# Kernel tuning notes

Hardware: AMD Instinct MI355X
Metric: run time of the kernel (lower is better)

Reference implementation:

```python
import jax, jax.numpy as jnp
import numpy as np

D = 512      # d_model
H = 8        # n_heads
DK = D // H  # head dim
DFF = 4 * D  # d_ff
E = 3        # encoder layers
PRED = 256   # pred_len
C_OUT = 64


def _ln(x, g, b):
    m = jnp.mean(x, axis=-1, keepdims=True)
    v = jnp.var(x, axis=-1, keepdims=True)
    return (x - m) / jnp.sqrt(v + 1e-5) * g + b


def _attn(q_in, kv_in, Wq, bq, Wk, bk, Wv, bv, Wo, bo, causal):
    B, L, _ = q_in.shape
    S = kv_in.shape[1]
    q = (q_in @ Wq + bq).reshape(B, L, H, DK)
    k = (kv_in @ Wk + bk).reshape(B, S, H, DK)
    v = (kv_in @ Wv + bv).reshape(B, S, H, DK)
    scores = jnp.einsum('blhe,bshe->bhls', q, k)  # [B,H,L,S]
    if causal:
        mask = jnp.triu(jnp.ones((L, S), dtype=bool), k=1)
        scores = jnp.where(mask, -jnp.inf, scores)
    scale = 1.0 / jnp.sqrt(jnp.asarray(DK, scores.dtype))
    A = jax.nn.softmax(scores * scale, axis=-1)
    out = jnp.einsum('bhls,bshd->blhd', A, v).reshape(B, L, H * DK)
    return out @ Wo + bo


def _gelu(x):
    return jax.nn.gelu(x, approximate=False)  # torch F.gelu is exact erf


def setup_inputs() -> dict:
    ks = iter(jax.random.split(jax.random.key(0), 80))
    r = lambda *s: jax.random.normal(next(ks), s, jnp.float32) * 0.02
    inp = {}
    inp['x_dec'] = jax.random.normal(next(ks), (8, 512, D), jnp.float32)
    inp['x_enc'] = jax.random.normal(next(ks), (8, 1024, D), jnp.float32)
    # encoder params, stacked over layers
    for nm in ['Wq', 'Wk', 'Wv', 'Wo']:
        inp[f'enc_{nm}'] = r(E, D, D)
        inp[f'enc_b{nm[1].lower()}'] = r(E, D)
    inp['enc_W1'] = r(E, D, DFF); inp['enc_b1'] = r(E, DFF)
    inp['enc_W2'] = r(E, DFF, D); inp['enc_b2'] = r(E, D)
    inp['enc_g1'] = jnp.ones((E, D)); inp['enc_beta1'] = jnp.zeros((E, D))
    inp['enc_g2'] = jnp.ones((E, D)); inp['enc_beta2'] = jnp.zeros((E, D))
    inp['enc_ng'] = jnp.ones((D,)); inp['enc_nbeta'] = jnp.zeros((D,))
    # decoder (single layer) params
    for p in ['s', 'c']:
        for nm in ['Wq', 'Wk', 'Wv', 'Wo']:
            inp[f'dec_{p}{nm}'] = r(D, D)
            inp[f'dec_{p}b{nm[1].lower()}'] = r(D)
    inp['dec_W1'] = r(D, DFF); inp['dec_b1'] = r(DFF)
    inp['dec_W2'] = r(DFF, D); inp['dec_b2'] = r(D)
    inp['dec_g1'] = jnp.ones((D,)); inp['dec_beta1'] = jnp.zeros((D,))
    inp['dec_g2'] = jnp.ones((D,)); inp['dec_beta2'] = jnp.zeros((D,))
    inp['dec_g3'] = jnp.ones((D,)); inp['dec_beta3'] = jnp.zeros((D,))
    inp['dec_ng'] = jnp.ones((D,)); inp['dec_nbeta'] = jnp.zeros((D,))
    inp['proj_W'] = r(D, C_OUT); inp['proj_b'] = r(C_OUT)
    return inp


def reference(x_dec, x_enc,
              enc_Wq, enc_bq, enc_Wk, enc_bk, enc_Wv, enc_bv, enc_Wo, enc_bo,
              enc_W1, enc_b1, enc_W2, enc_b2,
              enc_g1, enc_beta1, enc_g2, enc_beta2, enc_ng, enc_nbeta,
              dec_sWq, dec_sbq, dec_sWk, dec_sbk, dec_sWv, dec_sbv, dec_sWo, dec_sbo,
              dec_cWq, dec_cbq, dec_cWk, dec_cbk, dec_cWv, dec_cbv, dec_cWo, dec_cbo,
              dec_W1, dec_b1, dec_W2, dec_b2,
              dec_g1, dec_beta1, dec_g2, dec_beta2, dec_g3, dec_beta3,
              dec_ng, dec_nbeta, proj_W, proj_b):
    # ----- encoder (non-causal self-attn, eval mode: dropout = identity) -----
    x = x_enc
    for l in range(E):
        a = _attn(x, x, enc_Wq[l], enc_bq[l], enc_Wk[l], enc_bk[l],
                  enc_Wv[l], enc_bv[l], enc_Wo[l], enc_bo[l], causal=False)
        x = _ln(x + a, enc_g1[l], enc_beta1[l])
        y = _gelu(x @ enc_W1[l] + enc_b1[l]) @ enc_W2[l] + enc_b2[l]
        x = _ln(x + y, enc_g2[l], enc_beta2[l])
    enc_out = _ln(x, enc_ng, enc_nbeta)
    # ----- decoder (causal self-attn + cross-attn) -----
    x = x_dec
    a = _attn(x, x, dec_sWq, dec_sbq, dec_sWk, dec_sbk,
              dec_sWv, dec_sbv, dec_sWo, dec_sbo, causal=True)
    x = _ln(x + a, dec_g1, dec_beta1)
    a = _attn(x, enc_out, dec_cWq, dec_cbq, dec_cWk, dec_cbk,
              dec_cWv, dec_cbv, dec_cWo, dec_cbo, causal=False)
    x = _ln(x + a, dec_g2, dec_beta2)
    y = _gelu(x @ dec_W1 + dec_b1) @ dec_W2 + dec_b2
    x = _ln(x + y, dec_g3, dec_beta3)
    x = _ln(x, dec_ng, dec_nbeta)
    out = x @ proj_W + proj_b
    return out[:, -PRED:, :]
```

## Files before the change

### kernel.cpp

```cpp
#include <hip/hip_runtime.h>
#include <cstddef>

typedef __bf16 bf16;
typedef __bf16 bf16x8 __attribute__((ext_vector_type(8)));
typedef float f32x4 __attribute__((ext_vector_type(4)));

#define D 512
#define DFF 2048
#define MFMA __builtin_amdgcn_mfma_f32_16x16x32_bf16

__device__ __forceinline__ float load_any(const void* p, size_t i, int f) {
  return f ? ((const float*)p)[i] : (float)((const bf16*)p)[i];
}

__global__ void detect_dtype(const unsigned* __restrict__ x, int* flag) {
  __shared__ int cnt;
  if (threadIdx.x == 0) cnt = 0;
  __syncthreads();
  int local = 0;
  for (int i = threadIdx.x; i < 32768; i += 256) {
    unsigned e = (x[i] >> 7) & 0xFFu;
    if (e >= 160u) local++;
  }
  atomicAdd(&cnt, local);
  __syncthreads();
  if (threadIdx.x == 0) *flag = (cnt > 100) ? 1 : 0;
}

__global__ __launch_bounds__(256)
void conv_to_bf16(const void* __restrict__ src, bf16* __restrict__ dst, int n,
                  const int* __restrict__ flag) {
  const int f = *flag;
  for (int i = blockIdx.x * 256 + threadIdx.x; i < n; i += gridDim.x * 256)
    dst[i] = (bf16)load_any(src, i, f);
}

struct CDesc { const void* src; unsigned long long off; bf16* dst; int n; int pad; };
struct CPack { CDesc d[40]; };
__global__ __launch_bounds__(256)
void conv_batch(CPack P, const int* __restrict__ flag) {
  const CDesc& c = P.d[blockIdx.z];
  const int f = *flag;
  for (int i = blockIdx.x * 256 + threadIdx.x; i < c.n; i += gridDim.x * 256)
    c.dst[i] = (bf16)load_any(c.src, c.off + i, f);
}

struct TDesc { const void* src; unsigned long long off; bf16* dst; };
struct TPack { TDesc d[20]; };
__global__ __launch_bounds__(256)
void transpose_b(TPack P, int Kd, int Nd, const int* __restrict__ flag) {
  __shared__ bf16 tile[64][65];
  const TDesc& t = P.d[blockIdx.z];
  const int f = *flag;
  int tx = threadIdx.x & 63, ty = threadIdx.x >> 6;
  int nb = blockIdx.x * 64, kb = blockIdx.y * 64;
  #pragma unroll
  for (int r = ty; r < 64; r += 4)
    tile[r][tx] = (bf16)load_any(t.src, t.off + (size_t)(kb + r) * Nd + nb + tx, f);
  __syncthreads();
  #pragma unroll
  for (int r = ty; r < 64; r += 4)
    t.dst[(size_t)(nb + r) * Kd + kb + tx] = tile[tx][r];
}

__global__ __launch_bounds__(256)
void prep_kv(const bf16* __restrict__ K, const bf16* __restrict__ V,
             bf16* __restrict__ Kf, bf16* __restrict__ Vf, int S)
{
  __shared__ bf16 tile[64][72];
  const int kt = blockIdx.x, h = blockIdx.y, b = blockIdx.z;
  const int t = threadIdx.x;
  const int r = t >> 2, g = t & 3;
  const size_t srcrow = ((size_t)(b * S + kt * 64 + r)) * D + h * 64 + g * 16;
  const size_t bh = (size_t)(b * 8 + h);
  const size_t tbase = (bh * (S >> 6) + kt) * 4096;

  bf16x8 k0 = *(const bf16x8*)(K + srcrow);
  bf16x8 k1 = *(const bf16x8*)(K + srcrow + 8);
  const int nt = r >> 4, m15 = r & 15;
  const int c = g >> 1, qq = (g & 1) * 2;
  *(bf16x8*)(Kf + tbase + (((nt * 2 + c) * 64) + qq * 16 + m15) * 8)       = k0;
  *(bf16x8*)(Kf + tbase + (((nt * 2 + c) * 64) + (qq + 1) * 16 + m15) * 8) = k1;

  bf16x8 v0 = *(const bf16x8*)(V + srcrow);
  bf16x8 v1 = *(const bf16x8*)(V + srcrow + 8);
  #pragma unroll
  for (int u = 0; u < 8; u++) {
    tile[g * 16 + u][r]     = v0[u];
    tile[g * 16 + 8 + u][r] = v1[u];
  }
  __syncthreads();
  #pragma unroll
  for (int s = 0; s < 2; s++) {
    int i = t * 2 + s;
    int lane = i & 63, ntc = i >> 6;
    int vq = lane >> 4, vm = lane & 15;
    int vnt = ntc >> 1, vc = ntc & 1;
    bf16x8 o = *(const bf16x8*)(&tile[vnt * 16 + vm][vc * 32 + vq * 8]);
    *(bf16x8*)(Vf + tbase + (size_t)i * 8) = o;
  }
}

__device__ __forceinline__ void gload_lds16(const bf16* g, bf16* l) {
  __builtin_amdgcn_global_load_lds((const __attribute__((address_space(1))) void*)g,
                                   (__attribute__((address_space(3))) void*)l,
                                   16, 0, 0);
}

__global__ __launch_bounds__(256, 2)
void gemm_bt(const bf16* __restrict__ A, const bf16* __restrict__ BT,
             const bf16* __restrict__ bias, bf16* __restrict__ C,
             int M, int N, int K, int act)
{
  __shared__ bf16 As[128 * 32];
  __shared__ bf16 Bs[128 * 32];
  const int tid = threadIdx.x;
  const int bm = blockIdx.y, bn = blockIdx.x;
  const int wid = tid >> 6, lane = tid & 63;
  const int wm = (wid >> 1) << 6, wn = (wid & 1) << 6;
  const int l15 = lane & 15, q = lane >> 4;

  f32x4 acc[4][4] = {};

  const bf16* ag = A + (size_t)(bm * 128 + (tid >> 2)) * K + (tid & 3) * 8;
  const bf16* bg = BT + (size_t)(bn * 128 + (tid >> 2)) * K + (tid & 3) * 8;
  const size_t rstep = (size_t)64 * K;
  bf16* asl = As + tid * 8;
  bf16* bsl = Bs + tid * 8;

  for (int k0 = 0; k0 < K; k0 += 32) {
    __syncthreads();
    gload_lds16(ag + k0,          asl);
    gload_lds16(ag + k0 + rstep,  asl + 256 * 8);
    gload_lds16(bg + k0,          bsl);
    gload_lds16(bg + k0 + rstep,  bsl + 256 * 8);
    __syncthreads();

    bf16x8 af[4], bq[4];
    #pragma unroll
    for (int i = 0; i < 4; i++)
      af[i] = *(const bf16x8*)(As + (wm + i * 16 + l15) * 32 + q * 8);
    #pragma unroll
    for (int j = 0; j < 4; j++)
      bq[j] = *(const bf16x8*)(Bs + (wn + j * 16 + l15) * 32 + q * 8);
    #pragma unroll
    for (int i = 0; i < 4; i++)
      #pragma unroll
      for (int j = 0; j < 4; j++)
        acc[i][j] = MFMA(af[i], bq[j], acc[i][j], 0, 0, 0);
  }

  #pragma unroll
  for (int j = 0; j < 4; j++) {
    int gcol = bn * 128 + wn + j * 16 + l15;
    float bv = (float)bias[gcol];
    #pragma unroll
    for (int i = 0; i < 4; i++) {
      int grow = bm * 128 + wm + i * 16 + q * 4;
      #pragma unroll
      for (int r = 0; r < 4; r++) {
        float v = acc[i][j][r] + bv;
        if (act == 1) v = 0.5f * v * (1.0f + erff(v * 0.70710678118654752f));
        C[(size_t)(grow + r) * N + gcol] = (bf16)v;
      }
    }
  }
}

__global__ __launch_bounds__(256, 2)
void gemm_seg(const bf16* __restrict__ A, const bf16* __restrict__ BT,
              const bf16* __restrict__ bias,
              bf16* __restrict__ O0, bf16* __restrict__ O1, bf16* __restrict__ O2,
              int M, int K)
{
  __shared__ bf16 As[128 * 32];
  __shared__ bf16 Bs[128 * 32];
  const int tid = threadIdx.x;
  const int bm = blockIdx.y, bn = blockIdx.x;
  const int wid = tid >> 6, lane = tid & 63;
  const int wm = (wid >> 1) << 6, wn = (wid & 1) << 6;
  const int l15 = lane & 15, q = lane >> 4;

  f32x4 acc[4][4] = {};

  const bf16* ag = A + (size_t)(bm * 128 + (tid >> 2)) * K + (tid & 3) * 8;
  const bf16* bg = BT + (size_t)(bn * 128 + (tid >> 2)) * K + (tid & 3) * 8;
  const size_t rstep = (size_t)64 * K;
  bf16* asl = As + tid * 8;
  bf16* bsl = Bs + tid * 8;

  for (int k0 = 0; k0 < K; k0 += 32) {
    __syncthreads();
    gload_lds16(ag + k0,          asl);
    gload_lds16(ag + k0 + rstep,  asl + 256 * 8);
    gload_lds16(bg + k0,          bsl);
    gload_lds16(bg + k0 + rstep,  bsl + 256 * 8);
    __syncthreads();

    bf16x8 af[4], bq[4];
    #pragma unroll
    for (int i = 0; i < 4; i++)
      af[i] = *(const bf16x8*)(As + (wm + i * 16 + l15) * 32 + q * 8);
    #pragma unroll
    for (int j = 0; j < 4; j++)
      bq[j] = *(const bf16x8*)(Bs + (wn + j * 16 + l15) * 32 + q * 8);
    #pragma unroll
    for (int i = 0; i < 4; i++)
      #pragma unroll
      for (int j = 0; j < 4; j++)
        acc[i][j] = MFMA(af[i], bq[j], acc[i][j], 0, 0, 0);
  }

  const int seg = (bn * 128) >> 9;
  bf16* Cp = (seg == 0) ? O0 : ((seg == 1) ? O1 : O2);
  const int colb = seg << 9;

  #pragma unroll
  for (int j = 0; j < 4; j++) {
    int gcol = bn * 128 + wn + j * 16 + l15;
    float bv = (float)bias[gcol];
    int lcol = gcol - colb;
    #pragma unroll
    for (int i = 0; i < 4; i++) {
      int grow = bm * 128 + wm + i * 16 + q * 4;
      #pragma unroll
      for (int r = 0; r < 4; r++)
        Cp[(size_t)(grow + r) * 512 + lcol] = (bf16)(acc[i][j][r] + bv);
    }
  }
}

__global__ __launch_bounds__(256, 2)
void flash_attn(const bf16* __restrict__ Q, const bf16* __restrict__ Kf,
                const bf16* __restrict__ Vf, bf16* __restrict__ O,
                int L, int S, int causal)
{
  __shared__ bf16 PL[4][32 * 72];
  const int tid = threadIdx.x, wid = tid >> 6, lane = tid & 63;
  const int m15 = lane & 15, q = lane >> 4;
  const int b = blockIdx.z, h = blockIdx.y;
  const int wq = blockIdx.x * 128 + wid * 32;

  bf16x8 aq[2][2];
  #pragma unroll
  for (int qh = 0; qh < 2; qh++) {
    const bf16* qp = Q + ((size_t)(b * L + wq + qh * 16 + m15)) * D + h * 64 + q * 8;
    aq[qh][0] = *(const bf16x8*)(qp);
    aq[qh][1] = *(const bf16x8*)(qp + 32);
  }
  const size_t bh = (size_t)(b * 8 + h);
  const bf16* kfb = Kf + bh * ((size_t)S * 64);
  const bf16* vfb = Vf + bh * ((size_t)S * 64);

  f32x4 acco[2][4] = {};
  float ls[2][4] = {};

  const int ktmax = causal ? ((wq + 95) >> 6) : (S >> 6);

  bf16x8 kf[4][2];
  #pragma unroll
  for (int nt = 0; nt < 4; nt++)
    #pragma unroll
    for (int c = 0; c < 2; c++)
      kf[nt][c] = *(const bf16x8*)(kfb + ((nt * 2 + c) * 64 + lane) * 8);

  bf16* pl = &PL[wid][0];

  for (int kt = 0; kt < ktmax; kt++) {
    bf16x8 vf[4][2];
    const bf16* vc = vfb + (size_t)kt * 4096;
    #pragma unroll
    for (int nt = 0; nt < 4; nt++)
      #pragma unroll
      for (int c = 0; c < 2; c++)
        vf[nt][c] = *(const bf16x8*)(vc + ((nt * 2 + c) * 64 + lane) * 8);

    f32x4 sc[2][4];
    #pragma unroll
    for (int qh = 0; qh < 2; qh++)
      #pragma unroll
      for (int nt = 0; nt < 4; nt++) {
        f32x4 z = {};
        z = MFMA(aq[qh][0], kf[nt][0], z, 0, 0, 0);
        z = MFMA(aq[qh][1], kf[nt][1], z, 0, 0, 0);
        sc[qh][nt] = z;
      }

    {
      const int knext = (kt + 1 < ktmax) ? kt + 1 : kt;
      const bf16* kc = kfb + (size_t)knext * 4096;
      #pragma unroll
      for (int nt = 0; nt < 4; nt++)
        #pragma unroll
        for (int c = 0; c < 2; c++)
          kf[nt][c] = *(const bf16x8*)(kc + ((nt * 2 + c) * 64 + lane) * 8);
    }

    const bool mask = causal && (kt == ktmax - 1);
    #pragma unroll
    for (int qh = 0; qh < 2; qh++)
      #pragma unroll
      for (int nt = 0; nt < 4; nt++)
        #pragma unroll
        for (int r = 0; r < 4; r++) {
          float s = sc[qh][nt][r] * 0.125f;
          if (mask) {
            int kg = kt * 64 + nt * 16 + m15;
            int qg = wq + qh * 16 + q * 4 + r;
            if (kg > qg) s = -1e30f;
          }
          float p = __expf(s);
          ls[qh][r] += p;
          pl[(qh * 16 + q * 4 + r) * 72 + nt * 16 + m15] = (bf16)p;
        }

    #pragma unroll
    for (int qh = 0; qh < 2; qh++) {
      bf16x8 pa0 = *(const bf16x8*)(pl + (qh * 16 + m15) * 72 + q * 8);
      bf16x8 pa1 = *(const bf16x8*)(pl + (qh * 16 + m15) * 72 + 32 + q * 8);
      #pragma unroll
      for (int nt = 0; nt < 4; nt++) {
        acco[qh][nt] = MFMA(pa0, vf[nt][0], acco[qh][nt], 0, 0, 0);
        acco[qh][nt] = MFMA(pa1, vf[nt][1], acco[qh][nt], 0, 0, 0);
      }
    }
  }

  #pragma unroll
  for (int qh = 0; qh < 2; qh++)
    #pragma unroll
    for (int r = 0; r < 4; r++) {
      float v = ls[qh][r];
      v += __shfl_xor(v, 1); v += __shfl_xor(v, 2);
      v += __shfl_xor(v, 4); v += __shfl_xor(v, 8);
      ls[qh][r] = 1.0f / v;
    }

  #pragma unroll
  for (int qh = 0; qh < 2; qh++)
    #pragma unroll
    for (int nt = 0; nt < 4; nt++)
      #pragma unroll
      for (int r = 0; r < 4; r++)
        O[((size_t)(b * L + wq + qh * 16 + q * 4 + r)) * D + h * 64 + nt * 16 + m15] =
            (bf16)(acco[qh][nt][r] * ls[qh][r]);
}

__global__ __launch_bounds__(256)
void add_ln(const bf16* __restrict__ X, const bf16* __restrict__ R,
            const bf16* __restrict__ g, const bf16* __restrict__ be,
            bf16* __restrict__ Y, int hasR)
{
  __shared__ float red[4];
  const int row = blockIdx.x, tid = threadIdx.x;
  const bf16* x = X + (size_t)row * D;
  float v0 = (float)x[tid], v1 = (float)x[tid + 256];
  if (hasR) {
    const bf16* r = R + (size_t)row * D;
    v0 += (float)r[tid]; v1 += (float)r[tid + 256];
  }
  float s = v0 + v1;
  #pragma unroll
  for (int o = 32; o > 0; o >>= 1) s += __shfl_down(s, o);
  if ((tid & 63) == 0) red[tid >> 6] = s;
  __syncthreads();
  const float mean = (red[0] + red[1] + red[2] + red[3]) * (1.0f / 512.0f);
  __syncthreads();
  const float d0 = v0 - mean, d1 = v1 - mean;
  float sq = d0 * d0 + d1 * d1;
  #pragma unroll
  for (int o = 32; o > 0; o >>= 1) sq += __shfl_down(sq, o);
  if ((tid & 63) == 0) red[tid >> 6] = sq;
  __syncthreads();
  const float var = (red[0] + red[1] + red[2] + red[3]) * (1.0f / 512.0f);
  const float rstd = rsqrtf(var + 1e-5f);
  bf16* y = Y + (size_t)row * D;
  y[tid]       = (bf16)(d0 * rstd * (float)g[tid]       + (float)be[tid]);
  y[tid + 256] = (bf16)(d1 * rstd * (float)g[tid + 256] + (float)be[tid + 256]);
}

__global__ __launch_bounds__(256)
void proj_out(const bf16* __restrict__ X, const bf16* __restrict__ Wp,
              const bf16* __restrict__ bp, void* __restrict__ out,
              const int* __restrict__ flag)
{
  __shared__ float part[4][64];
  const int rb = blockIdx.x;
  const int b = rb >> 8, t = rb & 255;
  const int tid = threadIdx.x;
  const bf16* x = X + ((size_t)(b * 512 + 256 + t)) * D;
  const int c = tid & 63, seg = tid >> 6;
  float acc = 0.f;
  for (int k = seg * 128; k < seg * 128 + 128; k++)
    acc += (float)x[k] * (float)Wp[(size_t)k * 64 + c];
  part[seg][c] = acc;
  __syncthreads();
  if (tid < 64) {
    float v = part[0][tid] + part[1][tid] + part[2][tid] + part[3][tid] + (float)bp[tid];
    size_t idx = (size_t)rb * 64 + tid;
    if (*flag) ((float*)out)[idx] = v;
    else       ((bf16*)out)[idx] = (bf16)v;
  }
}

extern "C" void kernel_launch(void* const* d_in, const int* in_sizes, int n_in,
                              void* d_out, int out_size, void* d_ws, size_t ws_size,
                              hipStream_t stream)
{
  (void)in_sizes; (void)n_in; (void)out_size; (void)ws_size;

  char* wsb = (char*)d_ws;
  int* flag = (int*)wsb;
  bf16* w = (bf16*)(wsb + 256);
  size_t off = 0;
  auto alloc = [&](size_t n) { bf16* p = w + off; off += n; return p; };

  bf16* eQKVT = alloc(3 * (size_t)1536 * D);
  bf16* eWoT  = alloc(3 * (size_t)D * D);
  bf16* eW1T  = alloc(3 * (size_t)D * DFF);
  bf16* eW2T  = alloc(3 * (size_t)D * DFF);
  bf16* dQKVT = alloc((size_t)1536 * D);
  bf16* sWoT  = alloc((size_t)D * D);
  bf16* cWqT  = alloc((size_t)D * D);
  bf16* cKVT  = alloc((size_t)1024 * D);
  bf16* cWoT  = alloc((size_t)D * D);
  bf16* dW1T  = alloc((size_t)D * DFF);
  bf16* dW2T  = alloc((size_t)D * DFF);
  bf16* pW    = alloc((size_t)D * 64);
  bf16* e_qkvb  = alloc(3 * 1536);
  bf16* d_sqkvb = alloc(1536);
  bf16* d_ckvb  = alloc(1024);
  bf16* c_ebo = alloc(3 * D);
  bf16* c_eb1 = alloc(3 * DFF); bf16* c_eb2 = alloc(3 * D);
  bf16* c_eg1 = alloc(3 * D);   bf16* c_ebe1 = alloc(3 * D);
  bf16* c_eg2 = alloc(3 * D);   bf16* c_ebe2 = alloc(3 * D);
  bf16* c_eng = alloc(D);       bf16* c_enb = alloc(D);
  bf16* c_dsbo = alloc(D);
  bf16* c_dcbq = alloc(D);      bf16* c_dcbo = alloc(D);
  bf16* c_db1 = alloc(DFF);     bf16* c_db2 = alloc(D);
  bf16* c_dg1 = alloc(D);  bf16* c_dbe1 = alloc(D);
  bf16* c_dg2 = alloc(D);  bf16* c_dbe2 = alloc(D);
  bf16* c_dg3 = alloc(D);  bf16* c_dbe3 = alloc(D);
  bf16* c_dng = alloc(D);  bf16* c_dnb = alloc(D);
  bf16* c_pb  = alloc(64);
  bf16* xe   = alloc((size_t)8192 * D);
  bf16* enco = alloc((size_t)8192 * D);
  bf16* xd0  = alloc((size_t)4096 * D);
  bf16* xd   = alloc((size_t)4096 * D);
  bf16* qb   = alloc((size_t)8192 * D);
  bf16* kb   = alloc((size_t)8192 * D);
  bf16* vb   = alloc((size_t)8192 * D);
  bf16* t0   = alloc((size_t)8192 * D);
  bf16* t1   = alloc((size_t)8192 * D);
  bf16* mid  = qb;

  const dim3 tb(256);

  detect_dtype<<<dim3(1), tb, 0, stream>>>((const unsigned*)d_in[1], flag);

  conv_to_bf16<<<dim3(1024), tb, 0, stream>>>(d_in[1], xe, 8 * 1024 * D, flag);
  conv_to_bf16<<<dim3(1024), tb, 0, stream>>>(d_in[0], xd0, 8 * 512 * D, flag);

  {
    CPack P{};
    int n = 0;
    auto add = [&](int idx, unsigned long long o, bf16* dst, int cnt) {
      P.d[n++] = {d_in[idx], o, dst, cnt, 0};
    };
    add(9, 0, c_ebo, 1536);
    add(11, 0, c_eb1, 6144);  add(13, 0, c_eb2, 1536);
    add(14, 0, c_eg1, 1536);  add(15, 0, c_ebe1, 1536);
    add(16, 0, c_eg2, 1536);  add(17, 0, c_ebe2, 1536);
    add(18, 0, c_eng, 512);   add(19, 0, c_enb, 512);
    add(27, 0, c_dsbo, 512);
    add(29, 0, c_dcbq, 512);  add(35, 0, c_dcbo, 512);
    add(37, 0, c_db1, 2048);  add(39, 0, c_db2, 512);
    add(40, 0, c_dg1, 512);   add(41, 0, c_dbe1, 512);
    add(42, 0, c_dg2, 512);   add(43, 0, c_dbe2, 512);
    add(44, 0, c_dg3, 512);   add(45, 0, c_dbe3, 512);
    add(46, 0, c_dng, 512);   add(47, 0, c_dnb, 512);
    add(48, 0, pW, D * 64);   add(49, 0, c_pb, 64);
    for (int l = 0; l < 3; l++) {
      add(3, (unsigned long long)l * D, e_qkvb + l * 1536, 512);
      add(5, (unsigned long long)l * D, e_qkvb + l * 1536 + 512, 512);
      add(7, (unsigned long long)l * D, e_qkvb + l * 1536 + 1024, 512);
    }
    add(21, 0, d_sqkvb, 512); add(23, 0, d_sqkvb + 512, 512); add(25, 0, d_sqkvb + 1024, 512);
    add(31, 0, d_ckvb, 512);  add(33, 0, d_ckvb + 512, 512);
    conv_batch<<<dim3(24, 1, n), tb, 0, stream>>>(P, flag);
  }

  {
    TPack P{};
    int n = 0;
    for (int l = 0; l < 3; l++) {
      unsigned long long wo = (unsigned long long)l * D * D;
      bf16* dst = eQKVT + (size_t)l * 1536 * D;
      P.d[n++] = {d_in[2], wo, dst};
      P.d[n++] = {d_in[4], wo, dst + 512 * D};
      P.d[n++] = {d_in[6], wo, dst + 1024 * D};
      P.d[n++] = {d_in[8], wo, eWoT + wo};
    }
    P.d[n++] = {d_in[20], 0, dQKVT};
    P.d[n++] = {d_in[22], 0, dQKVT + 512 * D};
    P.d[n++] = {d_in[24], 0, dQKVT + 1024 * D};
    P.d[n++] = {d_in[26], 0, sWoT};
    P.d[n++] = {d_in[28], 0, cWqT};
    P.d[n++] = {d_in[30], 0, cKVT};
    P.d[n++] = {d_in[32], 0, cKVT + 512 * D};
    P.d[n++] = {d_in[34], 0, cWoT};
    transpose_b<<<dim3(8, 8, n), tb, 0, stream>>>(P, D, D, flag);
  }
  {
    TPack P{};
    for (int l = 0; l < 3; l++)
      P.d[l] = {d_in[10], (unsigned long long)l * D * DFF, eW1T + (size_t)l * D * DFF};
    P.d[3] = {d_in[36], 0, dW1T};
    transpose_b<<<dim3(32, 8, 4), tb, 0, stream>>>(P, D, DFF, flag);
  }
  {
    TPack P{};
    for (int l = 0; l < 3; l++)
      P.d[l] = {d_in[12], (unsigned long long)l * D * DFF, eW2T + (size_t)l * D * DFF};
    P.d[3] = {d_in[38], 0, dW2T};
    transpose_b<<<dim3(8, 32, 4), tb, 0, stream>>>(P, DFF, D, flag);
  }

  auto G = [&](const bf16* A, const bf16* BT, const bf16* bias, bf16* C,
               int M, int N, int K, int act) {
    gemm_bt<<<dim3(N / 128, M / 128), tb, 0, stream>>>(A, BT, bias, C, M, N, K, act);
  };
  auto GS = [&](const bf16* A, const bf16* BT, const bf16* bias,
                bf16* O0, bf16* O1, bf16* O2, int M, int N, int K) {
    gemm_seg<<<dim3(N / 128, M / 128), tb, 0, stream>>>(A, BT, bias, O0, O1, O2, M, K);
  };
  auto PK = [&](const bf16* Kp, const bf16* Vp, bf16* Kfp, bf16* Vfp, int S) {
    prep_kv<<<dim3(S / 64, 8, 8), tb, 0, stream>>>(Kp, Vp, Kfp, Vfp, S);
  };
  auto FA = [&](const bf16* Qp, const bf16* Kfp, const bf16* Vfp, bf16* Op,
                int L, int S, int causal) {
    flash_attn<<<dim3(L / 128, 8, 8), tb, 0, stream>>>(Qp, Kfp, Vfp, Op, L, S, causal);
  };

  const int Me = 8192;
  for (int l = 0; l < 3; l++) {
    const size_t wo = (size_t)l * D * D, fo = (size_t)l * D * DFF;
    GS(xe, eQKVT + (size_t)l * 1536 * D, e_qkvb + l * 1536, qb, kb, vb, Me, 1536, D);
    PK(kb, vb, t1, enco, 1024);
    FA(qb, t1, enco, t0, 1024, 1024, 0);
    G(t0, eWoT + wo, c_ebo + l * D, t1, Me, D, D, 0);
    add_ln<<<dim3(8192), tb, 0, stream>>>(t1, xe, c_eg1 + l * D, c_ebe1 + l * D, xe, 1);
    G(xe, eW1T + fo, c_eb1 + l * DFF, mid, Me, DFF, D, 1);
    G(mid, eW2T + fo, c_eb2 + l * D, t1, Me, D, DFF, 0);
    add_ln<<<dim3(8192), tb, 0, stream>>>(t1, xe, c_eg2 + l * D, c_ebe2 + l * D, xe, 1);
  }
  add_ln<<<dim3(8192), tb, 0, stream>>>(xe, nullptr, c_eng, c_enb, enco, 0);

  const int Md = 4096;
  GS(xd0, dQKVT, d_sqkvb, qb, kb, vb, Md, 1536, D);
  PK(kb, vb, t1, xd, 512);
  FA(qb, t1, xd, t0, 512, 512, 1);
  G(t0, sWoT, c_dsbo, t1, Md, D, D, 0);
  add_ln<<<dim3(4096), tb, 0, stream>>>(t1, xd0, c_dg1, c_dbe1, xd, 1);
  G(xd, cWqT, c_dcbq, qb, Md, D, D, 0);
  GS(enco, cKVT, d_ckvb, kb, vb, nullptr, Me, 1024, D);
  PK(kb, vb, t1, enco, 1024);
  FA(qb, t1, enco, t0, 512, 1024, 0);
  G(t0, cWoT, c_dcbo, t1, Md, D, D, 0);
  add_ln<<<dim3(4096), tb, 0, stream>>>(t1, xd, c_dg2, c_dbe2, xd, 1);
  G(xd, dW1T, c_db1, mid, Md, DFF, D, 1);
  G(mid, dW2T, c_db2, t1, Md, D, DFF, 0);
  add_ln<<<dim3(4096), tb, 0, stream>>>(t1, xd, c_dg3, c_dbe3, xd, 1);
  add_ln<<<dim3(4096), tb, 0, stream>>>(xd, nullptr, c_dng, c_dnb, xd, 0);
  proj_out<<<dim3(2048), tb, 0, stream>>>(xd, pW, c_pb, d_out, flag);
}
```

Baseline: 1.035 ms.

## Split-K for N=512 GEMMs with partial sums fused into add-LN, plus XCD block swizzle

Output-projection and FFN-down GEMMs (N=512) now use a two-way split-K kernel that writes two bf16 partial results. The add+layernorm kernel sums both partials, so no separate reduction pass is needed. The aim is to double the block count of these narrow GEMMs and fill more CUs. Separately, GEMM block indices are remapped so consecutive blocks spread across the 8 XCDs, to improve L2 reuse of A rows. The cost is an extra partial-buffer write and read per GEMM, and partials rounded to bf16 before summing slightly changes numerics.

Measured after the change: 950.9 us. 1.09x faster.

```diff
diff --git a/kernel.cpp b/kernel.cpp
--- a/kernel.cpp
+++ b/kernel.cpp
@@ -107,6 +107,17 @@
                                    16, 0, 0);
 }
 
+__device__ __forceinline__ void swizzle_bm_bn(int& bm, int& bn) {
+  int lin = blockIdx.y * gridDim.x + blockIdx.x;
+  if ((gridDim.y & 7) == 0) {
+    int xcd = lin & 7, j = lin >> 3;
+    bn = j % gridDim.x;
+    bm = xcd + 8 * (j / gridDim.x);
+  } else {
+    bn = blockIdx.x; bm = blockIdx.y;
+  }
+}
+
 __global__ __launch_bounds__(256, 2)
 void gemm_bt(const bf16* __restrict__ A, const bf16* __restrict__ BT,
              const bf16* __restrict__ bias, bf16* __restrict__ C,
@@ -115,7 +126,7 @@
   __shared__ bf16 As[128 * 32];
   __shared__ bf16 Bs[128 * 32];
   const int tid = threadIdx.x;
-  const int bm = blockIdx.y, bn = blockIdx.x;
+  int bm, bn; swizzle_bm_bn(bm, bn);
   const int wid = tid >> 6, lane = tid & 63;
   const int wm = (wid >> 1) << 6, wn = (wid & 1) << 6;
   const int l15 = lane & 15, q = lane >> 4;
@@ -168,6 +179,66 @@
 }
 
 __global__ __launch_bounds__(256, 2)
+void gemm_ks(const bf16* __restrict__ A, const bf16* __restrict__ BT,
+             const bf16* __restrict__ bias, bf16* __restrict__ P0,
+             bf16* __restrict__ P1, int M, int N, int K)
+{
+  __shared__ bf16 As[128 * 32];
+  __shared__ bf16 Bs[128 * 32];
+  const int tid = threadIdx.x;
+  int bm, bnl; swizzle_bm_bn(bm, bnl);
+  const int bn = bnl >> 1, split = bnl & 1;
+  const int Kh = K >> 1, kbase = split * Kh;
+  const int wid = tid >> 6, lane = tid & 63;
+  const int wm = (wid >> 1) << 6, wn = (wid & 1) << 6;
+  const int l15 = lane & 15, q = lane >> 4;
+
+  f32x4 acc[4][4] = {};
+
+  const bf16* ag = A + (size_t)(bm * 128 + (tid >> 2)) * K + kbase + (tid & 3) * 8;
+  const bf16* bg = BT + (size_t)(bn * 128 + (tid >> 2)) * K + kbase + (tid & 3) * 8;
+  const size_t rstep = (size_t)64 * K;
+  bf16* asl = As + tid * 8;
+  bf16* bsl = Bs + tid * 8;
+
+  for (int k0 = 0; k0 < Kh; k0 += 32) {
+    __syncthreads();
+    gload_lds16(ag + k0,          asl);
+    gload_lds16(ag + k0 + rstep,  asl + 256 * 8);
+    gload_lds16(bg + k0,          bsl);
+    gload_lds16(bg + k0 + rstep,  bsl + 256 * 8);
+    __syncthreads();
+
+    bf16x8 af[4], bq[4];
+    #pragma unroll
+    for (int i = 0; i < 4; i++)
+      af[i] = *(const bf16x8*)(As + (wm + i * 16 + l15) * 32 + q * 8);
+    #pragma unroll
+    for (int j = 0; j < 4; j++)
+      bq[j] = *(const bf16x8*)(Bs + (wn + j * 16 + l15) * 32 + q * 8);
+    #pragma unroll
+    for (int i = 0; i < 4; i++)
+      #pragma unroll
+      for (int j = 0; j < 4; j++)
+        acc[i][j] = MFMA(af[i], bq[j], acc[i][j], 0, 0, 0);
+  }
+
+  bf16* Cp = split ? P1 : P0;
+  #pragma unroll
+  for (int j = 0; j < 4; j++) {
+    int gcol = bn * 128 + wn + j * 16 + l15;
+    float bv = split ? 0.0f : (float)bias[gcol];
+    #pragma unroll
+    for (int i = 0; i < 4; i++) {
+      int grow = bm * 128 + wm + i * 16 + q * 4;
+      #pragma unroll
+      for (int r = 0; r < 4; r++)
+        Cp[(size_t)(grow + r) * 512 + gcol] = (bf16)(acc[i][j][r] + bv);
+    }
+  }
+}
+
+__global__ __launch_bounds__(256, 2)
 void gemm_seg(const bf16* __restrict__ A, const bf16* __restrict__ BT,
               const bf16* __restrict__ bias,
               bf16* __restrict__ O0, bf16* __restrict__ O1, bf16* __restrict__ O2,
@@ -176,7 +247,7 @@
   __shared__ bf16 As[128 * 32];
   __shared__ bf16 Bs[128 * 32];
   const int tid = threadIdx.x;
-  const int bm = blockIdx.y, bn = blockIdx.x;
+  int bm, bn; swizzle_bm_bn(bm, bn);
   const int wid = tid >> 6, lane = tid & 63;
   const int wm = (wid >> 1) << 6, wn = (wid & 1) << 6;
   const int l15 = lane & 15, q = lane >> 4;
@@ -347,14 +418,19 @@
 }
 
 __global__ __launch_bounds__(256)
-void add_ln(const bf16* __restrict__ X, const bf16* __restrict__ R,
+void add_ln(const bf16* __restrict__ X0, const bf16* __restrict__ X1,
+            const bf16* __restrict__ R,
             const bf16* __restrict__ g, const bf16* __restrict__ be,
             bf16* __restrict__ Y, int hasR)
 {
   __shared__ float red[4];
   const int row = blockIdx.x, tid = threadIdx.x;
-  const bf16* x = X + (size_t)row * D;
+  const bf16* x = X0 + (size_t)row * D;
   float v0 = (float)x[tid], v1 = (float)x[tid + 256];
+  if (X1 != nullptr) {
+    const bf16* p = X1 + (size_t)row * D;
+    v0 += (float)p[tid]; v1 += (float)p[tid + 256];
+  }
   if (hasR) {
     const bf16* r = R + (size_t)row * D;
     v0 += (float)r[tid]; v1 += (float)r[tid + 256];
@@ -530,6 +606,10 @@
                int M, int N, int K, int act) {
     gemm_bt<<<dim3(N / 128, M / 128), tb, 0, stream>>>(A, BT, bias, C, M, N, K, act);
   };
+  auto KS = [&](const bf16* A, const bf16* BT, const bf16* bias,
+                bf16* P0, bf16* P1, int M, int K) {
+    gemm_ks<<<dim3(8, M / 128), tb, 0, stream>>>(A, BT, bias, P0, P1, M, 512, K);
+  };
   auto GS = [&](const bf16* A, const bf16* BT, const bf16* bias,
                 bf16* O0, bf16* O1, bf16* O2, int M, int N, int K) {
     gemm_seg<<<dim3(N / 128, M / 128), tb, 0, stream>>>(A, BT, bias, O0, O1, O2, M, K);
@@ -541,6 +621,10 @@
                 int L, int S, int causal) {
     flash_attn<<<dim3(L / 128, 8, 8), tb, 0, stream>>>(Qp, Kfp, Vfp, Op, L, S, causal);
   };
+  auto LN = [&](const bf16* X0, const bf16* X1, const bf16* R,
+                const bf16* g, const bf16* be, bf16* Y, int hasR, int M) {
+    add_ln<<<dim3(M), tb, 0, stream>>>(X0, X1, R, g, be, Y, hasR);
+  };
 
   const int Me = 8192;
   for (int l = 0; l < 3; l++) {
@@ -548,29 +632,29 @@
     GS(xe, eQKVT + (size_t)l * 1536 * D, e_qkvb + l * 1536, qb, kb, vb, Me, 1536, D);
     PK(kb, vb, t1, enco, 1024);
     FA(qb, t1, enco, t0, 1024, 1024, 0);
-    G(t0, eWoT + wo, c_ebo + l * D, t1, Me, D, D, 0);
-    add_ln<<<dim3(8192), tb, 0, stream>>>(t1, xe, c_eg1 + l * D, c_ebe1 + l * D, xe, 1);
+    KS(t0, eWoT + wo, c_ebo + l * D, t1, enco, Me, 512);
+    LN(t1, enco, xe, c_eg1 + l * D, c_ebe1 + l * D, xe, 1, Me);
     G(xe, eW1T + fo, c_eb1 + l * DFF, mid, Me, DFF, D, 1);
-    G(mid, eW2T + fo, c_eb2 + l * D, t1, Me, D, DFF, 0);
-    add_ln<<<dim3(8192), tb, 0, stream>>>(t1, xe, c_eg2 + l * D, c_ebe2 + l * D, xe, 1);
-  }
-  add_ln<<<dim3(8192), tb, 0, stream>>>(xe, nullptr, c_eng, c_enb, enco, 0);
+    KS(mid, eW2T + fo, c_eb2 + l * D, t1, enco, Me, 2048);
+    LN(t1, enco, xe, c_eg2 + l * D, c_ebe2 + l * D, xe, 1, Me);
+  }
+  LN(xe, nullptr, nullptr, c_eng, c_enb, enco, 0, Me);
 
   const int Md = 4096;
   GS(xd0, dQKVT, d_sqkvb, qb, kb, vb, Md, 1536, D);
   PK(kb, vb, t1, xd, 512);
   FA(qb, t1, xd, t0, 512, 512, 1);
-  G(t0, sWoT, c_dsbo, t1, Md, D, D, 0);
-  add_ln<<<dim3(4096), tb, 0, stream>>>(t1, xd0, c_dg1, c_dbe1, xd, 1);
+  KS(t0, sWoT, c_dsbo, t1, vb, Md, 512);
+  LN(t1, vb, xd0, c_dg1, c_dbe1, xd, 1, Md);
   G(xd, cWqT, c_dcbq, qb, Md, D, D, 0);
   GS(enco, cKVT, d_ckvb, kb, vb, nullptr, Me, 1024, D);
   PK(kb, vb, t1, enco, 1024);
   FA(qb, t1, enco, t0, 512, 1024, 0);
-  G(t0, cWoT, c_dcbo, t1, Md, D, D, 0);
-  add_ln<<<dim3(4096), tb, 0, stream>>>(t1, xd, c_dg2, c_dbe2, xd, 1);
+  KS(t0, cWoT, c_dcbo, t1, vb, Md, 512);
+  LN(t1, vb, xd, c_dg2, c_dbe2, xd, 1, Md);
   G(xd, dW1T, c_db1, mid, Md, DFF, D, 1);
-  G(mid, dW2T, c_db2, t1, Md, D, DFF, 0);
-  add_ln<<<dim3(4096), tb, 0, stream>>>(t1, xd, c_dg3, c_dbe3, xd, 1);
-  add_ln<<<dim3(4096), tb, 0, stream>>>(xd, nullptr, c_dng, c_dnb, xd, 0);
+  KS(mid, dW2T, c_db2, t1, vb, Md, 2048);
+  LN(t1, vb, xd, c_dg3, c_dbe3, xd, 1, Md);
+  LN(xd, nullptr, nullptr, c_dng, c_dnb, xd, 0, Md);
   proj_out<<<dim3(2048), tb, 0, stream>>>(xd, pW, c_pb, d_out, flag);
 }
```
